# Optimization experiments

Measured on AMD Instinct MI355X. Metric: run time of the kernel, lower is better.

## Reference

```python
import jax, jax.numpy as jnp
import numpy as np

EPS = 1e-6
NUM_HEADS = 16  # config.num_attention_heads

def _rms(h, w):
    h32 = h.astype(jnp.float32)
    v = jnp.mean(h32 * h32, axis=-1, keepdims=True)
    return (w * h32 * jax.lax.rsqrt(v + EPS)).astype(h.dtype)

def _rope(q, k, pos):
    dh = q.shape[-1]
    inv = 1.0 / (10000.0 ** (jnp.arange(0, dh, 2, dtype=jnp.float32) / dh))
    ang = pos.astype(jnp.float32)[:, None] * inv[None, :]  # [n, dh/2]
    cos = jnp.concatenate([jnp.cos(ang), jnp.cos(ang)], -1)[None, None]  # [1,1,n,dh]
    sin = jnp.concatenate([jnp.sin(ang), jnp.sin(ang)], -1)[None, None]
    def rot(x):
        x1, x2 = x[..., :dh // 2], x[..., dh // 2:]
        return jnp.concatenate([-x2, x1], -1)
    return q * cos + rot(q) * sin, k * cos + rot(k) * sin

def _skip_causal_mask(N, block_size, len1, text_len):
    qi = jnp.arange(N)[:, None]
    ki = jnp.arange(N)[None, :]
    qb = (qi - text_len) // block_size
    kb = (ki - text_len) // block_size
    iq = qi >= text_len
    ik = ki >= text_len
    return (((ki < text_len) & (qi >= ki))
            | (iq & ik & (qb < len1) & (kb < len1) & (qb >= kb))
            | (iq & ik & (qb >= len1) & (kb < len1) & (qb - len1 > kb))
            | (iq & ik & (qb == kb)))

def _layer(x, position_ids, text_position_ids, qkv_w, qkv_b, proj_w, proj_b,
           qn_w, kn_w, ln1_w, ln2_w, gate_w, up_w, down_w,
           block_size, text_len, len1):
    B, N, C = x.shape
    H = NUM_HEADS
    Dh = C // H
    T = text_len
    Lc = len1 * block_size
    offs = [0, T, T + Lc]
    lens = [T, Lc, N - T - Lc]  # text / clean / noised segment lengths
    qs, ks, vs = [], [], []
    for i in range(3):
        seg = _rms(x[:, offs[i]:offs[i] + lens[i]], ln1_w[i])  # input layernorm
        qkv = seg @ qkv_w[i] + qkv_b[i]                        # [B,n,3C]
        qkv = qkv.reshape(B, lens[i], 3, H, Dh).transpose(2, 0, 3, 1, 4)
        qs.append(_rms(qkv[0], qn_w[i]))
        ks.append(_rms(qkv[1], kn_w[i]))
        vs.append(qkv[2])
    img_q = jnp.concatenate([qs[1], qs[2]], axis=2)
    img_k = jnp.concatenate([ks[1], ks[2]], axis=2)
    img_q, img_k = _rope(img_q, img_k, position_ids)
    txt_q, txt_k = _rope(qs[0], ks[0], text_position_ids)
    q = jnp.concatenate([txt_q, img_q], axis=2)
    k = jnp.concatenate([txt_k, img_k], axis=2)
    v = jnp.concatenate(vs, axis=2)
    scores = jnp.einsum('bhqd,bhkd->bhqk', q, k) / np.float32(np.sqrt(Dh))
    mask = _skip_causal_mask(N, block_size, len1, text_len)
    scores = jnp.where(mask, scores, jnp.finfo(scores.dtype).min)
    attn = jax.nn.softmax(scores, axis=-1)
    o = jnp.einsum('bhqk,bhkd->bhqd', attn, v)
    o = o.transpose(0, 2, 1, 3).reshape(B, N, C)
    o = jnp.concatenate([o[:, offs[i]:offs[i] + lens[i]] @ proj_w[i] + proj_b[i]
                         for i in range(3)], axis=1)
    h = x + o
    mlp = []
    for i in range(3):
        y = _rms(h[:, offs[i]:offs[i] + lens[i]], ln2_w[i])  # post-attn layernorm
        mlp.append((jax.nn.silu(y @ gate_w[i]) * (y @ up_w[i])) @ down_w[i])
    return h + jnp.concatenate(mlp, axis=1)

def setup_inputs():
    key = jax.random.key(0)
    ks = jax.random.split(key, 8)
    B, C, H, I = 2, 1024, 16, 4096
    block_size, text_len, len1, len2 = 128, 256, 4, 4
    N = text_len + (len1 + len2) * block_size  # 1280
    s = 0.02
    return {
        'x': jax.random.normal(ks[0], (B, N, C), jnp.float32),
        'position_ids': jnp.arange((len1 + len2) * block_size, dtype=jnp.int32),
        'text_position_ids': jnp.arange(text_len, dtype=jnp.int32),
        'qkv_w': jax.random.normal(ks[1], (3, C, 3 * C), jnp.float32) * s,
        'qkv_b': jnp.zeros((3, 3 * C), jnp.float32),
        'proj_w': jax.random.normal(ks[2], (3, C, C), jnp.float32) * s,
        'proj_b': jnp.zeros((3, C), jnp.float32),
        'qn_w': jnp.ones((3, C // H), jnp.float32),
        'kn_w': jnp.ones((3, C // H), jnp.float32),
        'ln1_w': jnp.ones((3, C), jnp.float32),
        'ln2_w': jnp.ones((3, C), jnp.float32),
        'gate_w': jax.random.normal(ks[3], (3, C, I), jnp.float32) * s,
        'up_w': jax.random.normal(ks[4], (3, C, I), jnp.float32) * s,
        'down_w': jax.random.normal(ks[5], (3, I, C), jnp.float32) * s,
        'block_size': block_size, 'text_len': text_len, 'len1': len1,
    }

def reference(x, position_ids, text_position_ids, qkv_w, qkv_b, proj_w, proj_b,
              qn_w, kn_w, ln1_w, ln2_w, gate_w, up_w, down_w,
              block_size, text_len, len1):
    return _layer(x, position_ids, text_position_ids, qkv_w, qkv_b, proj_w, proj_b,
                  qn_w, kn_w, ln1_w, ln2_w, gate_w, up_w, down_w,
                  block_size, text_len, len1)
```

## Files before the change

kernel.cpp:

```cpp
#include <hip/hip_runtime.h>
#include <math.h>

constexpr int Bb  = 2;
constexpr int Nn  = 1280;
constexpr int Cc  = 1024;
constexpr int Hh  = 16;
constexpr int DH  = 64;
constexpr int Ii  = 4096;
constexpr int Tt  = 256;
constexpr int BSz = 128;
constexpr int L1  = 4;
constexpr int Mrows = Bb * Nn;

typedef __attribute__((ext_vector_type(8))) short short8v;
typedef __attribute__((ext_vector_type(4))) float f32x4;

__device__ __forceinline__ int segof(int n) {
    return n < Tt ? 0 : (n < Tt + L1 * BSz ? 1 : 2);
}
__device__ __forceinline__ unsigned short f2bf(float f) {
    unsigned int u = __float_as_uint(f);
    u += 0x7fffu + ((u >> 16) & 1u);
    return (unsigned short)(u >> 16);
}
__device__ __forceinline__ float bf2f(unsigned short h) {
    return __uint_as_float(((unsigned int)h) << 16);
}

__device__ __forceinline__ int xcd_swz(int lin, int nwg) {
    int cpx = nwg >> 3;
    return (lin & 7) * cpx + (lin >> 3);
}

__device__ __forceinline__ void rms_dev(const float* __restrict__ in,
                                        const float* __restrict__ w,
                                        unsigned short* __restrict__ out,
                                        int row, float* sred) {
    int n   = row % Nn;
    int seg = segof(n);
    const float* x = in + (size_t)row * Cc;
    int t = threadIdx.x;
    float4 xv = reinterpret_cast<const float4*>(x)[t];
    float ss = xv.x * xv.x + xv.y * xv.y + xv.z * xv.z + xv.w * xv.w;
#pragma unroll
    for (int off = 32; off; off >>= 1) ss += __shfl_down(ss, off, 64);
    int lane = t & 63, wid = t >> 6;
    if (lane == 0) sred[wid] = ss;
    __syncthreads();
    if (t == 0) sred[4] = rsqrtf((sred[0] + sred[1] + sred[2] + sred[3]) * (1.0f / Cc) + 1e-6f);
    __syncthreads();
    float r = sred[4];
    float4 wv = reinterpret_cast<const float4*>(w + (size_t)seg * Cc)[t];
    ushort4 ov;
    ov.x = f2bf(wv.x * xv.x * r);
    ov.y = f2bf(wv.y * xv.y * r);
    ov.z = f2bf(wv.z * xv.z * r);
    ov.w = f2bf(wv.w * xv.w * r);
    *reinterpret_cast<ushort4*>(&out[(size_t)row * Cc + t * 4]) = ov;
}

__device__ __forceinline__ void pack_dev(const float* __restrict__ W,
                                         unsigned short* __restrict__ PB,
                                         int K, int Nd, size_t idx) {
    size_t cpseg = (size_t)K * Nd / 8;
    int s = (int)(idx / cpseg);
    size_t rm = idx % cpseg;
    int lane = (int)(rm & 63);
    int fr   = (int)((rm >> 6) & 7);
    size_t tile = rm >> 9;
    int nct = Nd >> 7;
    int cb = (int)(tile % nct);
    int kt = (int)(tile / nct);
    int col = cb * 128 + fr * 16 + (lane & 15);
    int k0  = kt * 32 + (lane >> 4) * 8;
    const float* src = W + ((size_t)s * K + k0) * Nd + col;
    unsigned short o[8];
#pragma unroll
    for (int j = 0; j < 8; j++) o[j] = f2bf(src[(size_t)j * Nd]);
    short8v v;
#pragma unroll
    for (int j = 0; j < 8; j++) v[j] = (short)o[j];
    *reinterpret_cast<short8v*>(&PB[idx * 8]) = v;
}

__global__ __launch_bounds__(256)
void pack_w(const float* __restrict__ W, unsigned short* __restrict__ PB,
            int K, int Nd) {
    pack_dev(W, PB, K, Nd, (size_t)blockIdx.x * 256 + threadIdx.x);
}

__global__ __launch_bounds__(256)
void fat1(const float* __restrict__ x, const float* __restrict__ ln1_w,
          unsigned short* __restrict__ xn,
          const float* __restrict__ qkv_w, unsigned short* __restrict__ qkv_p) {
    __shared__ float sred[5];
    int bid = blockIdx.x;
    if (bid < Mrows) {
        rms_dev(x, ln1_w, xn, bid, sred);
    } else {
        pack_dev(qkv_w, qkv_p, Cc, 3 * Cc, (size_t)(bid - Mrows) * 256 + threadIdx.x);
    }
}

__device__ __forceinline__ void attn_dev(
        const unsigned short* __restrict__ Qg, const unsigned short* __restrict__ Kg,
        const unsigned short* __restrict__ Vg, unsigned short* __restrict__ O,
        int qt, int bh,
        unsigned short* k_lds, unsigned short* vt_lds, unsigned short* p_base) {
    int b = bh >> 4, h = bh & 15;
    int tid = threadIdx.x, lane = tid & 63, wid = tid >> 6;
    int g = lane >> 4, c = lane & 15;

    const size_t headoff = (size_t)bh * Nn * DH;
    int q0 = qt * 64;
    bool qtext = q0 < Tt;
    int qb = qtext ? 0 : (q0 - Tt) / BSz;

    int qrow_frag = q0 + wid * 16 + c;
    short8v aq[2];
#pragma unroll
    for (int kb = 0; kb < 2; kb++)
        aq[kb] = *reinterpret_cast<const short8v*>(
            &Qg[headoff + (size_t)qrow_frag * DH + kb * 32 + g * 8]);

    unsigned short* pbuf = p_base + wid * 1024;

    f32x4 o_[4];
#pragma unroll
    for (int nb = 0; nb < 4; nb++) o_[nb] = (f32x4){0.f, 0.f, 0.f, 0.f};
    float m_[4] = {-3.4e38f, -3.4e38f, -3.4e38f, -3.4e38f};
    float l_[4] = {0.f, 0.f, 0.f, 0.f};

    int tr = tid >> 2, tc = tid & 3;

    for (int kt = 0; kt < Nn / 64; kt++) {
        int kbase = kt * 64;
        bool vis, diag = false;
        if (qtext) {
            vis = (kbase <= q0);
            diag = (kbase == q0);
        } else if (kbase < Tt) {
            vis = true;
        } else {
            int kb = (kbase - Tt) / BSz;
            vis = (qb < L1) ? (kb <= qb)
                            : ((kb < L1 && qb - L1 > kb) || kb == qb);
        }
        if (!vis) continue;

        __syncthreads();
        {
            const unsigned short* ks = &Kg[headoff + (size_t)(kbase + tr) * DH];
            const unsigned short* vs = &Vg[headoff + (size_t)(kbase + tr) * DH];
#pragma unroll
            for (int i = 0; i < 2; i++) {
                int ch = tc + i * 4;
                short8v kv = *reinterpret_cast<const short8v*>(ks + ch * 8);
                int byte = (tr * 128 + ch * 16) ^ ((tr & 7) << 4);
                *reinterpret_cast<short8v*>((char*)k_lds + byte) = kv;
                short8v vv = *reinterpret_cast<const short8v*>(vs + ch * 8);
#pragma unroll
                for (int j = 0; j < 8; j++) {
                    int dh = ch * 8 + j;
                    int vbyte = (dh * 128 + tr * 2) ^ ((dh & 7) << 4);
                    *reinterpret_cast<unsigned short*>((char*)vt_lds + vbyte) =
                        (unsigned short)vv[j];
                }
            }
        }
        __syncthreads();

        f32x4 s_[4];
#pragma unroll
        for (int nb = 0; nb < 4; nb++) s_[nb] = (f32x4){0.f, 0.f, 0.f, 0.f};
        __builtin_amdgcn_s_setprio(1);
#pragma unroll
        for (int nb = 0; nb < 4; nb++) {
            int kil = nb * 16 + c;
#pragma unroll
            for (int kb = 0; kb < 2; kb++) {
                int byte = (kil * 128 + kb * 64 + g * 16) ^ ((kil & 7) << 4);
                short8v bk = *reinterpret_cast<short8v*>((char*)k_lds + byte);
                s_[nb] = __builtin_amdgcn_mfma_f32_16x16x32_bf16(aq[kb], bk, s_[nb], 0, 0, 0);
            }
        }
        __builtin_amdgcn_s_setprio(0);
#pragma unroll
        for (int nb = 0; nb < 4; nb++) {
#pragma unroll
            for (int r = 0; r < 4; r++) {
                float sv = s_[nb][r] * 0.125f;
                if (diag) {
                    int qrl = wid * 16 + g * 4 + r;
                    int kcl = nb * 16 + c;
                    if (qrl < kcl) sv = -3.4e38f;
                }
                s_[nb][r] = sv;
            }
        }
#pragma unroll
        for (int r = 0; r < 4; r++) {
            float mx = fmaxf(fmaxf(s_[0][r], s_[1][r]), fmaxf(s_[2][r], s_[3][r]));
#pragma unroll
            for (int off = 1; off <= 8; off <<= 1)
                mx = fmaxf(mx, __shfl_xor(mx, off, 64));
            float mn = fmaxf(m_[r], mx);
            float es = __expf(m_[r] - mn);
            m_[r] = mn;
            float pv[4];
            float rs = 0.f;
#pragma unroll
            for (int nb = 0; nb < 4; nb++) {
                pv[nb] = __expf(s_[nb][r] - mn);
                rs += pv[nb];
            }
#pragma unroll
            for (int off = 1; off <= 8; off <<= 1)
                rs += __shfl_xor(rs, off, 64);
            l_[r] = l_[r] * es + rs;
#pragma unroll
            for (int nb = 0; nb < 4; nb++) o_[nb][r] *= es;
            int qrl = g * 4 + r;
            int swz = (qrl & 7) << 4;
#pragma unroll
            for (int nb = 0; nb < 4; nb++) {
                int byte = (qrl * 128 + (nb * 16 + c) * 2) ^ swz;
                *reinterpret_cast<unsigned short*>((char*)pbuf + byte) = f2bf(pv[nb]);
            }
        }
        short8v aP[2];
#pragma unroll
        for (int kb = 0; kb < 2; kb++) {
            int byte = (c * 128 + kb * 64 + g * 16) ^ ((c & 7) << 4);
            aP[kb] = *reinterpret_cast<short8v*>((char*)pbuf + byte);
        }
        __builtin_amdgcn_s_setprio(1);
#pragma unroll
        for (int nb = 0; nb < 4; nb++) {
            int dh = nb * 16 + c;
#pragma unroll
            for (int kb = 0; kb < 2; kb++) {
                int byte = (dh * 128 + kb * 64 + g * 16) ^ ((dh & 7) << 4);
                short8v bv = *reinterpret_cast<short8v*>((char*)vt_lds + byte);
                o_[nb] = __builtin_amdgcn_mfma_f32_16x16x32_bf16(aP[kb], bv, o_[nb], 0, 0, 0);
            }
        }
        __builtin_amdgcn_s_setprio(0);
    }

    float inv_[4];
#pragma unroll
    for (int r = 0; r < 4; r++) inv_[r] = 1.f / l_[r];
#pragma unroll
    for (int nb = 0; nb < 4; nb++) {
        int col = h * DH + nb * 16 + c;
#pragma unroll
        for (int r = 0; r < 4; r++) {
            int row = q0 + wid * 16 + g * 4 + r;
            O[((size_t)b * Nn + row) * Cc + col] = f2bf(o_[nb][r] * inv_[r]);
        }
    }
}

__global__ __launch_bounds__(256)
void fat2(const unsigned short* __restrict__ Qg, const unsigned short* __restrict__ Kg,
          const unsigned short* __restrict__ Vg, unsigned short* __restrict__ O,
          const float* __restrict__ proj_w, unsigned short* __restrict__ proj_p,
          const float* __restrict__ gate_w, unsigned short* __restrict__ gate_p,
          const float* __restrict__ up_w,   unsigned short* __restrict__ up_p) {
    __shared__ __align__(16) unsigned short k_lds[64 * 64];
    __shared__ __align__(16) unsigned short vt_lds[64 * 64];
    __shared__ __align__(16) unsigned short p_lds[4 * 16 * 64];
    int bid = blockIdx.x;
    if (bid < 640) {
        attn_dev(Qg, Kg, Vg, O, bid % 20, bid / 20, k_lds, vt_lds, p_lds);
        return;
    }
    bid -= 640;
    if (bid < 1536) {
        pack_dev(proj_w, proj_p, Cc, Cc, (size_t)bid * 256 + threadIdx.x);
        return;
    }
    bid -= 1536;
    if (bid < 6144) {
        pack_dev(gate_w, gate_p, Cc, Ii, (size_t)bid * 256 + threadIdx.x);
        return;
    }
    bid -= 6144;
    pack_dev(up_w, up_p, Cc, Ii, (size_t)bid * 256 + threadIdx.x);
}

template <int OUTMODE, bool BIAS, int NZ>
__global__ __launch_bounds__(256, 2)
void gemm128r(const unsigned short* __restrict__ A,
              const unsigned short* __restrict__ PB,
              const float* __restrict__ bias, void* __restrict__ outp,
              int K, int Nd) {
    __shared__ __align__(16) unsigned short lds[8192];
    int bx = blockIdx.x, by = blockIdx.y, bz = (NZ > 1) ? blockIdx.z : 0;
    {
        int gx = gridDim.x, gy = gridDim.y, gz = (NZ > 1) ? gridDim.z : 1;
        int lin = bx + gx * (by + gy * bz);
        int swz = xcd_swz(lin, gx * gy * gz);
        bx = swz % gx; swz /= gx;
        by = swz % gy; bz = swz / gy;
    }
    int rb = bx * 128, cb = by;
    int seg = segof(rb % Nn);
    int tid = threadIdx.x, lane = tid & 63, wid = tid >> 6;
    int wr = wid >> 1, wc = wid & 1;
    int g = lane >> 4, c_ = lane & 15;
    const int nct = Nd >> 7;
    const int Keff = K / NZ;
    const int nKt = Keff >> 5;
    const int kz = bz * Keff;
    const unsigned short* PBseg = PB + (size_t)seg * K * Nd;

    int mf0 = tid >> 6, lc0 = tid & 63;
    const unsigned short* pA0 =
        A + (size_t)(rb + mf0 * 16 + (lc0 & 15)) * K + kz + (lc0 >> 4) * 8;
    const unsigned short* pA1 = pA0 + (size_t)64 * K;
    const unsigned short* pB0 =
        PBseg + (((size_t)(kz >> 5) * nct + cb) * 8 + mf0) * 512 + (size_t)lc0 * 8;
    const unsigned short* pB1 = pB0 + 2048;
    const size_t bstep = (size_t)nct * 4096;

    f32x4 acc[4][4];
#pragma unroll
    for (int m = 0; m < 4; m++)
#pragma unroll
        for (int n = 0; n < 4; n++) acc[m][n] = (f32x4){0.f, 0.f, 0.f, 0.f};

    short8v avA0, avA1, bvA0, bvA1;
    short8v avB0, avB1, bvB0, bvB1;
    avA0 = *reinterpret_cast<const short8v*>(pA0);
    avA1 = *reinterpret_cast<const short8v*>(pA1);
    bvA0 = *reinterpret_cast<const short8v*>(pB0);
    bvA1 = *reinterpret_cast<const short8v*>(pB1);
    pA0 += 32; pA1 += 32; pB0 += bstep; pB1 += bstep;
    avB0 = *reinterpret_cast<const short8v*>(pA0);
    avB1 = *reinterpret_cast<const short8v*>(pA1);
    bvB0 = *reinterpret_cast<const short8v*>(pB0);
    bvB1 = *reinterpret_cast<const short8v*>(pB1);
    pA0 += 32; pA1 += 32; pB0 += bstep; pB1 += bstep;

    auto compute = [&]() {
        short8v afr[4], bfr[4];
#pragma unroll
        for (int m = 0; m < 4; m++)
            afr[m] = *reinterpret_cast<short8v*>(&lds[((wr * 4 + m) * 64 + lane) * 8]);
#pragma unroll
        for (int n = 0; n < 4; n++)
            bfr[n] = *reinterpret_cast<short8v*>(&lds[4096 + ((wc * 4 + n) * 64 + lane) * 8]);
#pragma unroll
        for (int m = 0; m < 4; m++)
#pragma unroll
            for (int n = 0; n < 4; n++)
                acc[m][n] = __builtin_amdgcn_mfma_f32_16x16x32_bf16(
                    afr[m], bfr[n], acc[m][n], 0, 0, 0);
    };

    for (int kt = 0; kt < nKt; kt += 2) {
        __syncthreads();
        *reinterpret_cast<short8v*>(&lds[(size_t)tid * 8]) = avA0;
        *reinterpret_cast<short8v*>(&lds[(size_t)(tid + 256) * 8]) = avA1;
        *reinterpret_cast<short8v*>(&lds[4096 + (size_t)tid * 8]) = bvA0;
        *reinterpret_cast<short8v*>(&lds[4096 + (size_t)(tid + 256) * 8]) = bvA1;
        __syncthreads();
        if (kt + 2 < nKt) {
            avA0 = *reinterpret_cast<const short8v*>(pA0);
            avA1 = *reinterpret_cast<const short8v*>(pA1);
            bvA0 = *reinterpret_cast<const short8v*>(pB0);
            bvA1 = *reinterpret_cast<const short8v*>(pB1);
            pA0 += 32; pA1 += 32; pB0 += bstep; pB1 += bstep;
        }
        compute();
        __syncthreads();
        *reinterpret_cast<short8v*>(&lds[(size_t)tid * 8]) = avB0;
        *reinterpret_cast<short8v*>(&lds[(size_t)(tid + 256) * 8]) = avB1;
        *reinterpret_cast<short8v*>(&lds[4096 + (size_t)tid * 8]) = bvB0;
        *reinterpret_cast<short8v*>(&lds[4096 + (size_t)(tid + 256) * 8]) = bvB1;
        __syncthreads();
        if (kt + 3 < nKt) {
            avB0 = *reinterpret_cast<const short8v*>(pA0);
            avB1 = *reinterpret_cast<const short8v*>(pA1);
            bvB0 = *reinterpret_cast<const short8v*>(pB0);
            bvB1 = *reinterpret_cast<const short8v*>(pB1);
            pA0 += 32; pA1 += 32; pB0 += bstep; pB1 += bstep;
        }
        compute();
    }

    float* outf = (float*)outp;
    unsigned short* outh = (unsigned short*)outp;
    size_t zoff = (NZ > 1) ? (size_t)bz * Mrows * Nd : 0;
#pragma unroll
    for (int n = 0; n < 4; n++) {
        int col = cb * 128 + wc * 64 + n * 16 + c_;
        float bvv = BIAS ? bias[(size_t)seg * Nd + col] : 0.f;
#pragma unroll
        for (int m = 0; m < 4; m++) {
#pragma unroll
            for (int r = 0; r < 4; r++) {
                int row = rb + wr * 64 + m * 16 + g * 4 + r;
                float v = acc[m][n][r] + bvv;
                if (OUTMODE == 0) outf[zoff + (size_t)row * Nd + col] = v;
                else              outh[zoff + (size_t)row * Nd + col] = f2bf(v);
            }
        }
    }
}

__global__ __launch_bounds__(256)
void gemm_gu(const unsigned short* __restrict__ A,
             const unsigned short* __restrict__ PG,
             const unsigned short* __restrict__ PU,
             unsigned short* __restrict__ outp) {
    __shared__ __align__(16) unsigned short lds[10240];
    int bx = blockIdx.x, by = blockIdx.y;
    {
        int lin = bx + gridDim.x * by;
        int swz = xcd_swz(lin, gridDim.x * gridDim.y);
        bx = swz % gridDim.x; by = swz / gridDim.x;
    }
    int rb = bx * 64, cb = by;
    int seg = segof(rb % Nn);
    int tid = threadIdx.x, lane = tid & 63, wid = tid >> 6;
    int wr = wid >> 1, wc = wid & 1;
    int g = lane >> 4, c_ = lane & 15;
    const int nct = Ii >> 7;
    const unsigned short* PGseg = PG + (size_t)seg * Cc * Ii;
    const unsigned short* PUseg = PU + (size_t)seg * Cc * Ii;

    f32x4 accG[2][4], accU[2][4];
#pragma unroll
    for (int m = 0; m < 2; m++)
#pragma unroll
        for (int n = 0; n < 4; n++) {
            accG[m][n] = (f32x4){0.f, 0.f, 0.f, 0.f};
            accU[m][n] = (f32x4){0.f, 0.f, 0.f, 0.f};
        }

    int mf0 = tid >> 6, lc0 = tid & 63;
    const unsigned short* gA =
        &A[(size_t)(rb + mf0 * 16 + (lc0 & 15)) * Cc + (lc0 >> 4) * 8];
    short8v av, gv[2], uv[2];
    auto load_tile = [&](int kt) {
        av = *reinterpret_cast<const short8v*>(gA + kt * 32);
#pragma unroll
        for (int i = 0; i < 2; i++) {
            int c = tid + i * 256;
            int cf = c >> 6, lc = c & 63;
            size_t off = (((size_t)kt * nct + cb) * 8 + cf) * 64 * 8 + (size_t)lc * 8;
            gv[i] = *reinterpret_cast<const short8v*>(PGseg + off);
            uv[i] = *reinterpret_cast<const short8v*>(PUseg + off);
        }
    };

    const int nKt = Cc >> 5;
    load_tile(0);
    for (int kt = 0; kt < nKt; ++kt) {
        __syncthreads();
        *reinterpret_cast<short8v*>(&lds[(size_t)tid * 8]) = av;
#pragma unroll
        for (int i = 0; i < 2; i++) {
            *reinterpret_cast<short8v*>(&lds[2048 + (size_t)(tid + i * 256) * 8]) = gv[i];
            *reinterpret_cast<short8v*>(&lds[6144 + (size_t)(tid + i * 256) * 8]) = uv[i];
        }
        __syncthreads();
        if (kt + 1 < nKt) load_tile(kt + 1);
        short8v afr[2], gfr[4], ufr[4];
#pragma unroll
        for (int m = 0; m < 2; m++)
            afr[m] = *reinterpret_cast<short8v*>(&lds[((wr * 2 + m) * 64 + lane) * 8]);
#pragma unroll
        for (int n = 0; n < 4; n++) {
            gfr[n] = *reinterpret_cast<short8v*>(&lds[2048 + ((wc * 4 + n) * 64 + lane) * 8]);
            ufr[n] = *reinterpret_cast<short8v*>(&lds[6144 + ((wc * 4 + n) * 64 + lane) * 8]);
        }
#pragma unroll
        for (int m = 0; m < 2; m++)
#pragma unroll
            for (int n = 0; n < 4; n++) {
                accG[m][n] = __builtin_amdgcn_mfma_f32_16x16x32_bf16(
                    afr[m], gfr[n], accG[m][n], 0, 0, 0);
                accU[m][n] = __builtin_amdgcn_mfma_f32_16x16x32_bf16(
                    afr[m], ufr[n], accU[m][n], 0, 0, 0);
            }
    }

#pragma unroll
    for (int n = 0; n < 4; n++) {
        int col = cb * 128 + wc * 64 + n * 16 + c_;
#pragma unroll
        for (int m = 0; m < 2; m++) {
#pragma unroll
            for (int r = 0; r < 4; r++) {
                int row = rb + wr * 32 + m * 16 + g * 4 + r;
                float gval = accG[m][n][r], uval = accU[m][n][r];
                float t = gval / (1.f + __expf(-gval)) * uval;
                outp[(size_t)row * Ii + col] = f2bf(t);
            }
        }
    }
}

__global__ __launch_bounds__(256)
void combine_rms(const float* __restrict__ x, const float* __restrict__ bias,
                 const unsigned short* __restrict__ p, const float* __restrict__ ln2_w,
                 float* __restrict__ out, unsigned short* __restrict__ y) {
    int row = blockIdx.x;
    int n   = row % Nn;
    int seg = segof(n);
    int t   = threadIdx.x;
    size_t i = (size_t)row * 256 + t;
    float4 a  = reinterpret_cast<const float4*>(x)[i];
    float4 b  = *reinterpret_cast<const float4*>(&bias[(size_t)seg * Cc + t * 4]);
    float4 h;
    h.x = a.x + b.x; h.y = a.y + b.y; h.z = a.z + b.z; h.w = a.w + b.w;
#pragma unroll
    for (int z = 0; z < 4; z++) {
        ushort4 u = *reinterpret_cast<const ushort4*>(&p[(size_t)z * Mrows * Cc + i * 4]);
        h.x += bf2f(u.x); h.y += bf2f(u.y); h.z += bf2f(u.z); h.w += bf2f(u.w);
    }
    reinterpret_cast<float4*>(out)[i] = h;
    float ss = h.x * h.x + h.y * h.y + h.z * h.z + h.w * h.w;
#pragma unroll
    for (int off = 32; off; off >>= 1) ss += __shfl_down(ss, off, 64);
    __shared__ float sred[5];
    int lane = t & 63, wid = t >> 6;
    if (lane == 0) sred[wid] = ss;
    __syncthreads();
    if (t == 0) sred[4] = rsqrtf((sred[0] + sred[1] + sred[2] + sred[3]) * (1.0f / Cc) + 1e-6f);
    __syncthreads();
    float r = sred[4];
    float4 wv = reinterpret_cast<const float4*>(ln2_w + (size_t)seg * Cc)[t];
    ushort4 ov;
    ov.x = f2bf(wv.x * h.x * r);
    ov.y = f2bf(wv.y * h.y * r);
    ov.z = f2bf(wv.z * h.z * r);
    ov.w = f2bf(wv.w * h.w * r);
    *reinterpret_cast<ushort4*>(&y[(size_t)row * Cc + t * 4]) = ov;
}

__global__ __launch_bounds__(256)
void combine_down4(const unsigned short* __restrict__ p,
                   float* __restrict__ out) {
    int i = blockIdx.x * 256 + threadIdx.x;
    float4 a = reinterpret_cast<const float4*>(out)[i];
#pragma unroll
    for (int z = 0; z < 4; z++) {
        ushort4 u = *reinterpret_cast<const ushort4*>(&p[(size_t)z * Mrows * Cc + i * 4]);
        a.x += bf2f(u.x); a.y += bf2f(u.y); a.z += bf2f(u.z); a.w += bf2f(u.w);
    }
    reinterpret_cast<float4*>(out)[i] = a;
}

__global__ __launch_bounds__(256)
void split_rope(const unsigned short* __restrict__ qkv,
                const float* __restrict__ qn_w, const float* __restrict__ kn_w,
                const int* __restrict__ pos_ids, const int* __restrict__ tpos_ids,
                unsigned short* __restrict__ Q, unsigned short* __restrict__ K,
                unsigned short* __restrict__ V) {
    int row = blockIdx.x;
    int b = row / Nn, n = row % Nn;
    int seg = segof(n);
    int lane = threadIdx.x & 63, wid = threadIdx.x >> 6;
    int pos = (n < Tt) ? tpos_ids[n] : pos_ids[n - Tt];
    int j = lane & 31;
    float ang = (float)pos * exp2f(-(float)j * (13.287712379549449f / 32.f));
    float cv = cosf(ang), sv = sinf(ang);
    float qw = qn_w[seg * DH + lane], kw = kn_w[seg * DH + lane];
    for (int h = wid; h < Hh; h += 4) {
        const unsigned short* base = qkv + (size_t)row * (3 * Cc) + h * DH + lane;
        float q = bf2f(base[0]), k = bf2f(base[Cc]), v = bf2f(base[2 * Cc]);
        float qs = q * q, ks = k * k;
#pragma unroll
        for (int off = 32; off; off >>= 1) {
            qs += __shfl_xor(qs, off, 64);
            ks += __shfl_xor(ks, off, 64);
        }
        q = q * rsqrtf(qs * (1.f / DH) + 1e-6f) * qw;
        k = k * rsqrtf(ks * (1.f / DH) + 1e-6f) * kw;
        float qp = __shfl_xor(q, 32, 64);
        float kp = __shfl_xor(k, 32, 64);
        float qo = q * cv + ((lane < 32) ? -qp * sv : qp * sv);
        float ko = k * cv + ((lane < 32) ? -kp * sv : kp * sv);
        size_t oidx = ((size_t)(b * Hh + h) * Nn + n) * DH + lane;
        Q[oidx] = f2bf(qo);
        K[oidx] = f2bf(ko);
        V[oidx] = f2bf(v);
    }
}

extern "C" void kernel_launch(void* const* d_in, const int* in_sizes, int n_in,
                              void* d_out, int out_size, void* d_ws, size_t ws_size,
                              hipStream_t stream) {
    const float* x        = (const float*)d_in[0];
    const int*   pos_ids  = (const int*)d_in[1];
    const int*   tpos_ids = (const int*)d_in[2];
    const float* qkv_w    = (const float*)d_in[3];
    const float* qkv_b    = (const float*)d_in[4];
    const float* proj_w   = (const float*)d_in[5];
    const float* proj_b   = (const float*)d_in[6];
    const float* qn_w     = (const float*)d_in[7];
    const float* kn_w     = (const float*)d_in[8];
    const float* ln1_w    = (const float*)d_in[9];
    const float* ln2_w    = (const float*)d_in[10];
    const float* gate_w   = (const float*)d_in[11];
    const float* up_w     = (const float*)d_in[12];
    const float* down_w   = (const float*)d_in[13];
    float* out = (float*)d_out;
    char*  wsb = (char*)d_ws;

    unsigned short* WA  = (unsigned short*)(wsb);
    unsigned short* WB  = (unsigned short*)(wsb + 25165824);
    unsigned short* Tb  = (unsigned short*)(wsb + 50331648);
    unsigned short* P3  = (unsigned short*)(wsb + 71303168);
    unsigned short* P4  = (unsigned short*)(wsb + 76546048);
    unsigned short* Qbf = Tb;
    unsigned short* Kbf = Tb + 2621440;
    unsigned short* Vbf = Tb + 5242880;

    fat1<<<Mrows + 4608, 256, 0, stream>>>(x, ln1_w, P3, qkv_w, WA);
    gemm128r<1, true, 1><<<dim3(Mrows / 128, 24), 256, 0, stream>>>(
        P3, WA, qkv_b, WB, Cc, 3 * Cc);
    split_rope<<<Mrows, 256, 0, stream>>>(WB, qn_w, kn_w, pos_ids, tpos_ids,
                                          Qbf, Kbf, Vbf);
    fat2<<<640 + 1536 + 6144 + 6144, 256, 0, stream>>>(
        Qbf, Kbf, Vbf, P3, proj_w, P4, gate_w, WA, up_w, WB);
    gemm128r<1, false, 4><<<dim3(Mrows / 128, 8, 4), 256, 0, stream>>>(
        P3, P4, nullptr, Tb, Cc, Cc);
    combine_rms<<<Mrows, 256, 0, stream>>>(x, proj_b, Tb, ln2_w, out, P3);
    gemm_gu<<<dim3(Mrows / 64, 32), 256, 0, stream>>>(P3, WA, WB, Tb);
    pack_w<<<6144, 256, 0, stream>>>(down_w, WA, Ii, Cc);
    gemm128r<1, false, 4><<<dim3(Mrows / 128, 8, 4), 256, 0, stream>>>(
        Tb, WA, nullptr, WB, Ii, Cc);
    combine_down4<<<Mrows * Cc / 1024, 256, 0, stream>>>(WB, out);
}
```

Before: 242.1 us.

## Fuse QK RMS norm, RoPE and head split into QKV GEMM epilogue

Replaces the generic QKV GEMM plus separate split_rope kernel with a dedicated GEMM whose epilogue applies the per-head RMS norm, RoPE and head-major scatter directly from registers. The RoPE cos/sin table is precomputed by extra blocks appended to the fat1 launch, and it is stored in the P4 buffer before fat2 overwrites it. This removes one launch and the bf16 QKV intermediate write and reread. The cost is a heavier epilogue with shuffles and scattered 2-byte stores.

New measurement: 233.7 us. 3.5% less time.

```diff
diff --git a/kernel.cpp b/kernel.cpp
--- a/kernel.cpp
+++ b/kernel.cpp
@@ -92,14 +92,26 @@
 __global__ __launch_bounds__(256)
 void fat1(const float* __restrict__ x, const float* __restrict__ ln1_w,
           unsigned short* __restrict__ xn,
-          const float* __restrict__ qkv_w, unsigned short* __restrict__ qkv_p) {
+          const float* __restrict__ qkv_w, unsigned short* __restrict__ qkv_p,
+          const int* __restrict__ pos_ids, const int* __restrict__ tpos_ids,
+          float2* __restrict__ tab) {
     __shared__ float sred[5];
     int bid = blockIdx.x;
     if (bid < Mrows) {
         rms_dev(x, ln1_w, xn, bid, sred);
-    } else {
-        pack_dev(qkv_w, qkv_p, Cc, 3 * Cc, (size_t)(bid - Mrows) * 256 + threadIdx.x);
-    }
+        return;
+    }
+    bid -= Mrows;
+    if (bid < 4608) {
+        pack_dev(qkv_w, qkv_p, Cc, 3 * Cc, (size_t)bid * 256 + threadIdx.x);
+        return;
+    }
+    bid -= 4608;
+    int idx = bid * 256 + threadIdx.x;
+    int n = idx >> 5, j = idx & 31;
+    int pos = (n < Tt) ? tpos_ids[n] : pos_ids[n - Tt];
+    float ang = (float)pos * exp2f(-(float)j * (13.287712379549449f / 32.f));
+    tab[idx] = make_float2(cosf(ang), sinf(ang));
 }
 
 __device__ __forceinline__ void attn_dev(
@@ -406,6 +418,169 @@
                 float v = acc[m][n][r] + bvv;
                 if (OUTMODE == 0) outf[zoff + (size_t)row * Nd + col] = v;
                 else              outh[zoff + (size_t)row * Nd + col] = f2bf(v);
+            }
+        }
+    }
+}
+
+__global__ __launch_bounds__(256, 2)
+void gemm_qkv(const unsigned short* __restrict__ A,
+              const unsigned short* __restrict__ PB,
+              const float* __restrict__ bias,
+              const float* __restrict__ qn_w, const float* __restrict__ kn_w,
+              const float2* __restrict__ tab,
+              unsigned short* __restrict__ Q, unsigned short* __restrict__ K,
+              unsigned short* __restrict__ V) {
+    __shared__ __align__(16) unsigned short lds[8192];
+    const int Kd = Cc, Nd = 3 * Cc;
+    int bx = blockIdx.x, by = blockIdx.y;
+    {
+        int lin = bx + gridDim.x * by;
+        int swz = xcd_swz(lin, gridDim.x * gridDim.y);
+        bx = swz % gridDim.x; by = swz / gridDim.x;
+    }
+    int rb = bx * 128, cb = by;
+    int seg = segof(rb % Nn);
+    int tid = threadIdx.x, lane = tid & 63, wid = tid >> 6;
+    int wr = wid >> 1, wc = wid & 1;
+    int g = lane >> 4, c_ = lane & 15;
+    const int nct = Nd >> 7;
+    const int nKt = Kd >> 5;
+    const unsigned short* PBseg = PB + (size_t)seg * Kd * Nd;
+
+    int mf0 = tid >> 6, lc0 = tid & 63;
+    const unsigned short* pA0 =
+        A + (size_t)(rb + mf0 * 16 + (lc0 & 15)) * Kd + (lc0 >> 4) * 8;
+    const unsigned short* pA1 = pA0 + (size_t)64 * Kd;
+    const unsigned short* pB0 =
+        PBseg + (((size_t)cb) * 8 + mf0) * 512 + (size_t)lc0 * 8;
+    const unsigned short* pB1 = pB0 + 2048;
+    const size_t bstep = (size_t)nct * 4096;
+
+    f32x4 acc[4][4];
+#pragma unroll
+    for (int m = 0; m < 4; m++)
+#pragma unroll
+        for (int n = 0; n < 4; n++) acc[m][n] = (f32x4){0.f, 0.f, 0.f, 0.f};
+
+    short8v avA0, avA1, bvA0, bvA1;
+    short8v avB0, avB1, bvB0, bvB1;
+    avA0 = *reinterpret_cast<const short8v*>(pA0);
+    avA1 = *reinterpret_cast<const short8v*>(pA1);
+    bvA0 = *reinterpret_cast<const short8v*>(pB0);
+    bvA1 = *reinterpret_cast<const short8v*>(pB1);
+    pA0 += 32; pA1 += 32; pB0 += bstep; pB1 += bstep;
+    avB0 = *reinterpret_cast<const short8v*>(pA0);
+    avB1 = *reinterpret_cast<const short8v*>(pA1);
+    bvB0 = *reinterpret_cast<const short8v*>(pB0);
+    bvB1 = *reinterpret_cast<const short8v*>(pB1);
+    pA0 += 32; pA1 += 32; pB0 += bstep; pB1 += bstep;
+
+    auto compute = [&]() {
+        short8v afr[4], bfr[4];
+#pragma unroll
+        for (int m = 0; m < 4; m++)
+            afr[m] = *reinterpret_cast<short8v*>(&lds[((wr * 4 + m) * 64 + lane) * 8]);
+#pragma unroll
+        for (int n = 0; n < 4; n++)
+            bfr[n] = *reinterpret_cast<short8v*>(&lds[4096 + ((wc * 4 + n) * 64 + lane) * 8]);
+#pragma unroll
+        for (int m = 0; m < 4; m++)
+#pragma unroll
+            for (int n = 0; n < 4; n++)
+                acc[m][n] = __builtin_amdgcn_mfma_f32_16x16x32_bf16(
+                    afr[m], bfr[n], acc[m][n], 0, 0, 0);
+    };
+
+    for (int kt = 0; kt < nKt; kt += 2) {
+        __syncthreads();
+        *reinterpret_cast<short8v*>(&lds[(size_t)tid * 8]) = avA0;
+        *reinterpret_cast<short8v*>(&lds[(size_t)(tid + 256) * 8]) = avA1;
+        *reinterpret_cast<short8v*>(&lds[4096 + (size_t)tid * 8]) = bvA0;
+        *reinterpret_cast<short8v*>(&lds[4096 + (size_t)(tid + 256) * 8]) = bvA1;
+        __syncthreads();
+        if (kt + 2 < nKt) {
+            avA0 = *reinterpret_cast<const short8v*>(pA0);
+            avA1 = *reinterpret_cast<const short8v*>(pA1);
+            bvA0 = *reinterpret_cast<const short8v*>(pB0);
+            bvA1 = *reinterpret_cast<const short8v*>(pB1);
+            pA0 += 32; pA1 += 32; pB0 += bstep; pB1 += bstep;
+        }
+        compute();
+        __syncthreads();
+        *reinterpret_cast<short8v*>(&lds[(size_t)tid * 8]) = avB0;
+        *reinterpret_cast<short8v*>(&lds[(size_t)(tid + 256) * 8]) = avB1;
+        *reinterpret_cast<short8v*>(&lds[4096 + (size_t)tid * 8]) = bvB0;
+        *reinterpret_cast<short8v*>(&lds[4096 + (size_t)(tid + 256) * 8]) = bvB1;
+        __syncthreads();
+        if (kt + 3 < nKt) {
+            avB0 = *reinterpret_cast<const short8v*>(pA0);
+            avB1 = *reinterpret_cast<const short8v*>(pA1);
+            bvB0 = *reinterpret_cast<const short8v*>(pB0);
+            bvB1 = *reinterpret_cast<const short8v*>(pB1);
+            pA0 += 32; pA1 += 32; pB0 += bstep; pB1 += bstep;
+        }
+        compute();
+    }
+
+    int colbase = cb * 128 + wc * 64;
+    int three = colbase >> 10;
+    int h = (colbase & 1023) >> 6;
+    float bv[4];
+#pragma unroll
+    for (int n = 0; n < 4; n++)
+        bv[n] = bias[(size_t)seg * (3 * Cc) + colbase + n * 16 + c_];
+
+    if (three == 2) {
+#pragma unroll
+        for (int m = 0; m < 4; m++) {
+#pragma unroll
+            for (int r = 0; r < 4; r++) {
+                int grow = rb + wr * 64 + m * 16 + g * 4 + r;
+                int b = (grow >= Nn) ? 1 : 0;
+                int nrow = grow - b * Nn;
+                size_t base = ((size_t)(b * Hh + h) * Nn + nrow) * DH;
+#pragma unroll
+                for (int n = 0; n < 4; n++)
+                    V[base + n * 16 + c_] = f2bf(acc[m][n][r] + bv[n]);
+            }
+        }
+        return;
+    }
+
+    const float* nwp = (three == 0 ? qn_w : kn_w) + (size_t)seg * DH;
+    float nwv[4];
+#pragma unroll
+    for (int n = 0; n < 4; n++) nwv[n] = nwp[n * 16 + c_];
+    unsigned short* outT = (three == 0) ? Q : K;
+
+#pragma unroll
+    for (int m = 0; m < 4; m++) {
+#pragma unroll
+        for (int r = 0; r < 4; r++) {
+            int grow = rb + wr * 64 + m * 16 + g * 4 + r;
+            int b = (grow >= Nn) ? 1 : 0;
+            int nrow = grow - b * Nn;
+            float val[4];
+#pragma unroll
+            for (int n = 0; n < 4; n++) val[n] = acc[m][n][r] + bv[n];
+            float ss = val[0] * val[0] + val[1] * val[1] +
+                       val[2] * val[2] + val[3] * val[3];
+#pragma unroll
+            for (int off = 1; off <= 8; off <<= 1)
+                ss += __shfl_xor(ss, off, 64);
+            float rn = rsqrtf(ss * (1.f / DH) + 1e-6f);
+#pragma unroll
+            for (int n = 0; n < 4; n++) val[n] *= rn * nwv[n];
+            size_t base = ((size_t)(b * Hh + h) * Nn + nrow) * DH;
+#pragma unroll
+            for (int n = 0; n < 2; n++) {
+                int j = n * 16 + c_;
+                float2 cs = tab[(size_t)nrow * 32 + j];
+                float lo = val[n] * cs.x - val[n + 2] * cs.y;
+                float hi = val[n + 2] * cs.x + val[n] * cs.y;
+                outT[base + n * 16 + c_]        = f2bf(lo);
+                outT[base + (n + 2) * 16 + c_]  = f2bf(hi);
             }
         }
     }
@@ -554,43 +729,6 @@
         a.x += bf2f(u.x); a.y += bf2f(u.y); a.z += bf2f(u.z); a.w += bf2f(u.w);
     }
     reinterpret_cast<float4*>(out)[i] = a;
-}
-
-__global__ __launch_bounds__(256)
-void split_rope(const unsigned short* __restrict__ qkv,
-                const float* __restrict__ qn_w, const float* __restrict__ kn_w,
-                const int* __restrict__ pos_ids, const int* __restrict__ tpos_ids,
-                unsigned short* __restrict__ Q, unsigned short* __restrict__ K,
-                unsigned short* __restrict__ V) {
-    int row = blockIdx.x;
-    int b = row / Nn, n = row % Nn;
-    int seg = segof(n);
-    int lane = threadIdx.x & 63, wid = threadIdx.x >> 6;
-    int pos = (n < Tt) ? tpos_ids[n] : pos_ids[n - Tt];
-    int j = lane & 31;
-    float ang = (float)pos * exp2f(-(float)j * (13.287712379549449f / 32.f));
-    float cv = cosf(ang), sv = sinf(ang);
-    float qw = qn_w[seg * DH + lane], kw = kn_w[seg * DH + lane];
-    for (int h = wid; h < Hh; h += 4) {
-        const unsigned short* base = qkv + (size_t)row * (3 * Cc) + h * DH + lane;
-        float q = bf2f(base[0]), k = bf2f(base[Cc]), v = bf2f(base[2 * Cc]);
-        float qs = q * q, ks = k * k;
-#pragma unroll
-        for (int off = 32; off; off >>= 1) {
-            qs += __shfl_xor(qs, off, 64);
-            ks += __shfl_xor(ks, off, 64);
-        }
-        q = q * rsqrtf(qs * (1.f / DH) + 1e-6f) * qw;
-        k = k * rsqrtf(ks * (1.f / DH) + 1e-6f) * kw;
-        float qp = __shfl_xor(q, 32, 64);
-        float kp = __shfl_xor(k, 32, 64);
-        float qo = q * cv + ((lane < 32) ? -qp * sv : qp * sv);
-        float ko = k * cv + ((lane < 32) ? -kp * sv : kp * sv);
-        size_t oidx = ((size_t)(b * Hh + h) * Nn + n) * DH + lane;
-        Q[oidx] = f2bf(qo);
-        K[oidx] = f2bf(ko);
-        V[oidx] = f2bf(v);
-    }
 }
 
 extern "C" void kernel_launch(void* const* d_in, const int* in_sizes, int n_in,
@@ -621,12 +759,12 @@
     unsigned short* Qbf = Tb;
     unsigned short* Kbf = Tb + 2621440;
     unsigned short* Vbf = Tb + 5242880;
-
-    fat1<<<Mrows + 4608, 256, 0, stream>>>(x, ln1_w, P3, qkv_w, WA);
-    gemm128r<1, true, 1><<<dim3(Mrows / 128, 24), 256, 0, stream>>>(
-        P3, WA, qkv_b, WB, Cc, 3 * Cc);
-    split_rope<<<Mrows, 256, 0, stream>>>(WB, qn_w, kn_w, pos_ids, tpos_ids,
-                                          Qbf, Kbf, Vbf);
+    float2*         tab = (float2*)P4;
+
+    fat1<<<Mrows + 4608 + 160, 256, 0, stream>>>(x, ln1_w, P3, qkv_w, WA,
+                                                 pos_ids, tpos_ids, tab);
+    gemm_qkv<<<dim3(Mrows / 128, 24), 256, 0, stream>>>(
+        P3, WA, qkv_b, qn_w, kn_w, tab, Qbf, Kbf, Vbf);
     fat2<<<640 + 1536 + 6144 + 6144, 256, 0, stream>>>(
         Qbf, Kbf, Vbf, P3, proj_w, P4, gate_w, WA, up_w, WB);
     gemm128r<1, false, 4><<<dim3(Mrows / 128, 8, 4), 256, 0, stream>>>(
```
